# Kernel tuning notes

Hardware: AMD Instinct MI355X
Metric: run time of the kernel (lower is better)

The kernel has to match this reference:

```python
import jax, jax.numpy as jnp
import numpy as np

B = 8192
FL = 96      # feature_len
K = 3        # dynamic filter kernel size
NOUT = 2
EPS = 1e-5
P = (K - 1) // 2

def _lrelu(x):
    return jnp.where(x >= 0, x, 0.1 * x)

def _conv1d(x, w, b):
    # x: [b,1,L], w: [1,1,3], b: [1]; padding=1, stride=1
    y = jax.lax.conv_general_dilated(x, w, (1,), [(1, 1)], dimension_numbers=('NCH', 'OIH', 'NCH'))
    return y + b[None, :, None]

def _bn(y, g, be, m, v):
    # eval-mode BatchNorm1d with running stats
    return (y - m) / jnp.sqrt(v + EPS) * g + be


def setup_inputs() -> dict:
    key = jax.random.key(0)
    ks = jax.random.split(key, 40)
    d = {'x': jax.random.normal(ks[0], (B, 576), jnp.float32)}
    # trans_layer: 6 conv1d (1->1, k=3)
    for i in range(6):
        d[f'cw{i+1}'] = jax.random.normal(ks[1 + i], (1, 1, 3), jnp.float32) * 0.4
        d[f'cb{i+1}'] = jax.random.normal(ks[7 + i], (1,), jnp.float32) * 0.1
    # fusion_layer.de_dimen: Linear(FL -> K*K)
    d['de_W'] = jax.random.normal(ks[13], (K * K, FL), jnp.float32) * 0.1
    d['de_b'] = jnp.zeros((K * K,), jnp.float32)
    # reshape_layer: Linear(2*FL -> 3*FL) + BN
    d['rs_W'] = jax.random.normal(ks[14], (3 * FL, 2 * FL), jnp.float32) * 0.07
    d['rs_b'] = jnp.zeros((3 * FL,), jnp.float32)
    d['rs_g'] = 1.0 + 0.1 * jax.random.normal(ks[15], (3 * FL,), jnp.float32)
    d['rs_be'] = 0.1 * jax.random.normal(ks[16], (3 * FL,), jnp.float32)
    d['rs_m'] = 0.05 * jax.random.normal(ks[17], (3 * FL,), jnp.float32)
    d['rs_v'] = jax.random.uniform(ks[18], (3 * FL,), jnp.float32, 0.5, 1.5)
    # classifier_shallow: Linear(6*FL -> 3*FL) + BN + ReLU + Linear(3*FL -> NOUT)
    d['cl_W1'] = jax.random.normal(ks[19], (3 * FL, 6 * FL), jnp.float32) * 0.05
    d['cl_b1'] = jnp.zeros((3 * FL,), jnp.float32)
    d['cl_g'] = 1.0 + 0.1 * jax.random.normal(ks[20], (3 * FL,), jnp.float32)
    d['cl_be'] = 0.1 * jax.random.normal(ks[21], (3 * FL,), jnp.float32)
    d['cl_m'] = 0.05 * jax.random.normal(ks[22], (3 * FL,), jnp.float32)
    d['cl_v'] = jax.random.uniform(ks[23], (3 * FL,), jnp.float32, 0.5, 1.5)
    d['cl_W2'] = jax.random.normal(ks[24], (NOUT, 3 * FL), jnp.float32) * 0.05
    d['cl_b2'] = jnp.zeros((NOUT,), jnp.float32)
    return d


def reference(x, cw1, cb1, cw2, cb2, cw3, cb3, cw4, cb4, cw5, cb5, cw6, cb6,
              de_W, de_b, rs_W, rs_b, rs_g, rs_be, rs_m, rs_v,
              cl_W1, cl_b1, cl_g, cl_be, cl_m, cl_v, cl_W2, cl_b2):
    def trans(c):  # c: [b,1,3*FL] -> three [b,1,FL]
        s1, s2, s3 = c[..., :FL], c[..., FL:2 * FL], c[..., 2 * FL:]
        x1 = _lrelu(_conv1d(s1, cw1, cb1))
        x2 = _lrelu(_conv1d(s2, cw2, cb2))
        x3 = _lrelu(_conv1d(s3, cw3, cb3))
        return (_lrelu(_conv1d(x1, cw4, cb4)),
                _lrelu(_conv1d(x2, cw5, cb5)),
                _lrelu(_conv1d(x3, cw6, cb6)))

    def fusion(arm, x86, bert):  # each [b,1,FL]
        b = arm.shape[0]
        # c==1 so matmul(s_1^T, s_2) is a per-sample outer product: [b,FL,FL]
        m = _lrelu(jnp.einsum('bl,bm->blm', arm[:, 0], x86[:, 0]))
        # per-sample 3x3 dynamic filter from bert embedding
        s3 = _lrelu(bert[:, 0] @ de_W.T + de_b).reshape(b, 1, K, K)
        fe = jax.lax.conv_general_dilated(
            m.reshape(1, b, FL, FL), s3, (1, 1), [(P, P), (P, P)],
            feature_group_count=b, dimension_numbers=('NCHW', 'OIHW', 'NCHW'))
        fe = _lrelu(fe).reshape(b, FL, FL)
        # AvgPool1d(FL) == mean over last dim (and over rows for the permuted map)
        return jnp.concatenate([fe.mean(axis=2), fe.mean(axis=1)], axis=1)  # [b,2*FL]

    def resh(e):
        return _lrelu(_bn(e @ rs_W.T + rs_b, rs_g, rs_be, rs_m, rs_v))

    xu = x[:, None, :]  # unsqueeze(dim=1)
    c1, c2 = xu[..., :3 * FL], xu[..., 3 * FL:]
    e1 = resh(fusion(*trans(c1))) + c1[:, 0]
    e2 = resh(fusion(*trans(c2))) + c2[:, 0]
    ce = jnp.concatenate([e1, e2], axis=1)  # [b,6*FL]
    # Dropout is identity in eval mode
    h = jax.nn.relu(_bn(ce @ cl_W1.T + cl_b1, cl_g, cl_be, cl_m, cl_v))
    return h @ cl_W2.T + cl_b2  # [b,NOUT]
```

## Files before the change

kernel.cpp:

```cpp
#include <hip/hip_runtime.h>
#include <hip/hip_bf16.h>
#include <math.h>

#define FLn 96
#define SEG 288
#define EPRE_DIM 192
#define EPS_BN 1e-5f

typedef __attribute__((ext_vector_type(8))) short short8;
typedef __attribute__((ext_vector_type(4))) float floatx4;
typedef float v2f __attribute__((ext_vector_type(2)));

__device__ __forceinline__ float lrelu(float v) { return fmaxf(v, 0.1f * v); }
__device__ __forceinline__ short f2bf(float f) {
  __hip_bfloat16 h = __float2bfloat16(f);
  return *reinterpret_cast<short*>(&h);
}

#define O_CIN 0
#define O_ST1 288
#define O_APP 576
#define O_ANP 674
#define O_XPP 772
#define O_XNP 870
#define O_BERT 968
#define O_WKER 1064
#define O_ABF 0
#define O_BBF 384
#define O_RP 0
#define RPREG 1632
#define SLICE 3264

__global__ __launch_bounds__(128) void k1_persample(
    const float* __restrict__ x,
    const float* __restrict__ cw1, const float* __restrict__ cb1,
    const float* __restrict__ cw2, const float* __restrict__ cb2,
    const float* __restrict__ cw3, const float* __restrict__ cb3,
    const float* __restrict__ cw4, const float* __restrict__ cb4,
    const float* __restrict__ cw5, const float* __restrict__ cb5,
    const float* __restrict__ cw6, const float* __restrict__ cb6,
    const float* __restrict__ deW, const float* __restrict__ deb,
    const float* __restrict__ rsW, const float* __restrict__ clW1,
    short* __restrict__ wB2s, short* __restrict__ wB3s,
    short* __restrict__ epre_s) {
  __shared__ float S[SLICE];
  short* Ssh = (short*)S;
  const int tid = threadIdx.x;
  const int sw = tid >> 6;
  const int lane = tid & 63;
  const int quad = lane >> 4;
  const int l16 = lane & 15;
  const int unit = blockIdx.x;
  const float* xrow = x + (size_t)(unit >> 1) * 576 + (unit & 1) * 288;

  {
    int d = blockIdx.x * 128 + tid;
    if (d < 18 * 6 * 512) {
      int j = d & 7, ln = (d >> 3) & 63, t = d >> 9;
      int kf = t % 6, nf = t / 6;
      int n = nf * 16 + (ln & 15);
      int k = kf * 32 + (ln >> 4) * 8 + j;
      wB2s[d] = f2bf(rsW[n * 192 + k]);
    }
    if (d < 18 * 18 * 512) {
      int j = d & 7, ln = (d >> 3) & 63, t = d >> 9;
      int kf = t % 18, nt = t / 18;
      int n = nt * 16 + (ln & 15);
      int k = kf * 32 + (ln >> 4) * 8 + j;
      wB3s[d] = f2bf(clW1[n * 576 + k]);
    }
  }

  const float a0w0 = cw1[0], a0w1 = cw1[1], a0w2 = cw1[2], a0b = cb1[0];
  const float a1w0 = cw2[0], a1w1 = cw2[1], a1w2 = cw2[2], a1b = cb2[0];
  const float a2w0 = cw3[0], a2w1 = cw3[1], a2w2 = cw3[2], a2b = cb3[0];
  const float b0w0 = cw4[0], b0w1 = cw4[1], b0w2 = cw4[2], b0b = cb4[0];
  const float b1w0 = cw5[0], b1w1 = cw5[1], b1w2 = cw5[2], b1b = cb5[0];
  const float b2w0 = cw6[0], b2w1 = cw6[1], b2w2 = cw6[2], b2b = cb6[0];

  for (int t4 = tid; t4 < 72; t4 += 128)
    *(float4*)&S[O_CIN + 4 * t4] = ((const float4*)xrow)[t4];
  if (tid < 8) S[576 + 98 * (tid >> 1) + (tid & 1) * 97] = 0.f;
  __syncthreads();

  for (int t = tid; t < SEG; t += 128) {
    bool g1 = t >= 96, g2 = t >= 192;
    float wa = g2 ? a2w0 : (g1 ? a1w0 : a0w0);
    float wb = g2 ? a2w1 : (g1 ? a1w1 : a0w1);
    float wc = g2 ? a2w2 : (g1 ? a1w2 : a0w2);
    float bb = g2 ? a2b  : (g1 ? a1b  : a0b);
    int p = t - (g2 ? 192 : (g1 ? 96 : 0));
    float l = p > 0 ? S[O_CIN + t - 1] : 0.f;
    float m = S[O_CIN + t];
    float r = p < FLn - 1 ? S[O_CIN + t + 1] : 0.f;
    S[O_ST1 + t] = lrelu(fmaf(wa, l, fmaf(wb, m, fmaf(wc, r, bb))));
  }
  __syncthreads();
  for (int t = tid; t < SEG; t += 128) {
    bool g1 = t >= 96, g2 = t >= 192;
    float wa = g2 ? b2w0 : (g1 ? b1w0 : b0w0);
    float wb = g2 ? b2w1 : (g1 ? b1w1 : b0w1);
    float wc = g2 ? b2w2 : (g1 ? b1w2 : b0w2);
    float bb = g2 ? b2b  : (g1 ? b1b  : b0b);
    int p = t - (g2 ? 192 : (g1 ? 96 : 0));
    float l = p > 0 ? S[O_ST1 + t - 1] : 0.f;
    float m = S[O_ST1 + t];
    float r = p < FLn - 1 ? S[O_ST1 + t + 1] : 0.f;
    float v = lrelu(fmaf(wa, l, fmaf(wb, m, fmaf(wc, r, bb))));
    if (!g1) {
      S[O_APP + 1 + p] = fmaxf(v, 0.1f * v);
      S[O_ANP + 1 + p] = fminf(v, 0.1f * v);
    } else if (!g2) {
      S[O_XPP + 1 + p] = fmaxf(v, 0.f);
      S[O_XNP + 1 + p] = fminf(v, 0.f);
    } else {
      S[O_BERT + p] = v;
    }
  }
  __syncthreads();

  if (sw == 0) {
    if (quad < 3) {
      float bv[6];
#pragma unroll
      for (int k = 0; k < 6; ++k) bv[k] = S[O_BERT + l16 + 16 * k];
#pragma unroll
      for (int oi = 0; oi < 3; ++oi) {
        int o = quad * 3 + oi;
        float p = 0.f;
#pragma unroll
        for (int k = 0; k < 6; ++k) p = fmaf(bv[k], deW[o * 96 + l16 + 16 * k], p);
        p += __shfl_xor(p, 1, 16);
        p += __shfl_xor(p, 2, 16);
        p += __shfl_xor(p, 4, 16);
        p += __shfl_xor(p, 8, 16);
        if (l16 == 0) S[O_WKER + o] = lrelu(p + deb[o]);
      }
    }
  } else {
    for (int m = lane; m < 96; m += 64) {
      short8 a;
      a[0] = f2bf(S[O_APP + m]);
      a[1] = f2bf(S[O_APP + m + 1]);
      a[2] = f2bf(S[O_APP + m + 2]);
      a[3] = f2bf(S[O_ANP + m]);
      a[4] = f2bf(S[O_ANP + m + 1]);
      a[5] = f2bf(S[O_ANP + m + 2]);
      a[6] = 0; a[7] = 0;
      *(short8*)&Ssh[2 * O_ABF + m * 8] = a;
    }
  }
  __syncthreads();

  {
    float w9[9];
#pragma unroll
    for (int q = 0; q < 9; ++q) w9[q] = 0.25f * S[O_WKER + q];
    for (int t = tid; t < 96; t += 128) {
      float xp0 = S[O_XPP + t], xp1 = S[O_XPP + t + 1], xp2 = S[O_XPP + t + 2];
      float xn0 = S[O_XNP + t], xn1 = S[O_XNP + t + 1], xn2 = S[O_XNP + t + 2];
      short8 b;
#pragma unroll
      for (int d = 0; d < 3; ++d) {
        float cp = fmaf(w9[3 * d], xp0, fmaf(w9[3 * d + 1], xp1, w9[3 * d + 2] * xp2));
        float cn = fmaf(w9[3 * d], xn0, fmaf(w9[3 * d + 1], xn1, w9[3 * d + 2] * xn2));
        b[d] = f2bf(cp);
        b[3 + d] = f2bf(cn);
      }
      b[6] = 0; b[7] = 0;
      *(short8*)&Ssh[2 * O_BBF + t * 8] = b;
    }
  }
  __syncthreads();

  short8 aF[6];
#pragma unroll
  for (int mt = 0; mt < 6; ++mt)
    aF[mt] = *(const short8*)&Ssh[2 * O_ABF + (mt * 16 + l16) * 8];

  v2f rp2[6][2];
#pragma unroll
  for (int mt = 0; mt < 6; ++mt) {
    rp2[mt][0] = (v2f){0.f, 0.f};
    rp2[mt][1] = (v2f){0.f, 0.f};
  }
  float cs[3];

#pragma unroll
  for (int si = 0; si < 3; ++si) {
    const int s = 3 * sw + si;
    short8 bF = *(const short8*)&Ssh[2 * O_BBF + (s * 16 + l16) * 8];
    floatx4 accv[6];
#pragma unroll
    for (int mt = 0; mt < 6; ++mt)
      accv[mt] = __builtin_amdgcn_mfma_f32_16x16x32_bf16(
          aF[mt], bF, (floatx4){0.f, 0.f, 0.f, 0.f}, 0, 0, 0);
    v2f csl = (v2f){0.f, 0.f};
#pragma unroll
    for (int mt = 0; mt < 6; ++mt) {
      v2f lo = (v2f){accv[mt][0], accv[mt][1]};
      v2f hi = (v2f){accv[mt][2], accv[mt][3]};
      v2f tl = 0.1f * lo;
      v2f th = 0.1f * hi;
      v2f fl, fh;
      fl.x = fmaxf(lo.x, tl.x); fl.y = fmaxf(lo.y, tl.y);
      fh.x = fmaxf(hi.x, th.x); fh.y = fmaxf(hi.y, th.y);
      rp2[mt][0] += fl;
      rp2[mt][1] += fh;
      csl += fl + fh;
    }
    cs[si] = csl.x + csl.y;
  }
  __syncthreads();

#pragma unroll
  for (int mt = 0; mt < 6; ++mt)
    *(float4*)&S[O_RP + sw * RPREG + (quad * 6 + mt) * 68 + l16 * 4] =
        make_float4(rp2[mt][0].x, rp2[mt][0].y, rp2[mt][1].x, rp2[mt][1].y);
  __syncthreads();

  const int g = unit >> 4;
  const int u15 = unit & 15;
  short* eb = epre_s + (size_t)g * 6 * 512;
  for (int i = tid; i < 96; i += 128) {
    int gg = ((i >> 2) & 3) * 6 + (i >> 4);
    int r = i & 3;
    float s = 0.f;
#pragma unroll
    for (int l = 0; l < 16; ++l)
      s += S[O_RP + gg * 68 + l * 4 + r] + S[O_RP + RPREG + gg * 68 + l * 4 + r];
    int kf = i >> 5, rem = i & 31, q = rem >> 3, j = rem & 7;
    eb[kf * 512 + (q * 16 + u15) * 8 + j] = f2bf(s * (1.f / FLn));
  }
#pragma unroll
  for (int si = 0; si < 3; ++si) {
    float v = cs[si];
    v += __shfl_xor(v, 16, 64);
    v += __shfl_xor(v, 32, 64);
    if (quad == 0) {
      int kidx = 96 + (3 * sw + si) * 16 + l16;
      int kf = kidx >> 5, rem = kidx & 31, q = rem >> 3, j = rem & 7;
      eb[kf * 512 + (q * 16 + u15) * 8 + j] = f2bf(v * (1.f / FLn));
    }
  }
}

__global__ __launch_bounds__(512) void k6_fused_tail(
    const short* __restrict__ epre_s, const short* __restrict__ wB2s,
    const short* __restrict__ wB3s, const float* __restrict__ x,
    const float* __restrict__ rsb, const float* __restrict__ rsg,
    const float* __restrict__ rsbe, const float* __restrict__ rsm,
    const float* __restrict__ rsv,
    const float* __restrict__ clb1, const float* __restrict__ clg,
    const float* __restrict__ clbe, const float* __restrict__ clm,
    const float* __restrict__ clv,
    const float* __restrict__ clW2, const float* __restrict__ clb2,
    float* __restrict__ out) {
  __shared__ short ceT[16 * 584];
  __shared__ float scr[8 * 32];
  const int tid = threadIdx.x;
  const int w = tid >> 6;
  const int lane = tid & 63;
  const int quad = lane >> 4;
  const int l16 = lane & 15;
  const int s0 = blockIdx.x * 16;

  const int mt = w & 1;
  const int ng = w >> 1;
  short8 aF[6];
  {
    const short* arow = epre_s + (size_t)(blockIdx.x * 2 + mt) * 6 * 512 + lane * 8;
#pragma unroll
    for (int kf = 0; kf < 6; ++kf) aF[kf] = *(const short8*)(arow + kf * 512);
  }

  for (int nf = ng; nf < 18; nf += 4) {
    const short* brow = wB2s + (size_t)nf * 6 * 512 + lane * 8;
    floatx4 acc = (floatx4){0.f, 0.f, 0.f, 0.f};
#pragma unroll
    for (int kf = 0; kf < 6; ++kf) {
      short8 bF = *(const short8*)(brow + kf * 512);
      acc = __builtin_amdgcn_mfma_f32_16x16x32_bf16(aF[kf], bF, acc, 0, 0, 0);
    }
    const int n = nf * 16 + l16;
    const float sc = rsg[n] * rsqrtf(rsv[n] + EPS_BN);
    const float vb = rsb[n], mu = rsm[n], vbe = rsbe[n];
#pragma unroll
    for (int r = 0; r < 4; ++r) {
      int um = mt * 16 + quad * 4 + r;
      int trow = um >> 1;
      int cc = (um & 1) * 288 + n;
      float y = acc[r] + vb;
      float o = (y - mu) * sc + vbe;
      float e = lrelu(o) + x[(size_t)(s0 + trow) * 576 + cc];
      ceT[trow * 584 + cc] = f2bf(e);
    }
  }
  __syncthreads();

  float p0[4], p1[4];
#pragma unroll
  for (int r = 0; r < 4; ++r) { p0[r] = 0.f; p1[r] = 0.f; }

  for (int nt = w; nt < 18; nt += 8) {
    const short* brow = wB3s + (size_t)nt * 18 * 512 + lane * 8;
    floatx4 acc = (floatx4){0.f, 0.f, 0.f, 0.f};
#pragma unroll
    for (int kf = 0; kf < 18; ++kf) {
      short8 cF = *(const short8*)&ceT[l16 * 584 + kf * 32 + quad * 8];
      short8 bF = *(const short8*)(brow + kf * 512);
      acc = __builtin_amdgcn_mfma_f32_16x16x32_bf16(cF, bF, acc, 0, 0, 0);
    }
    const int n = nt * 16 + l16;
    const float sc = clg[n] * rsqrtf(clv[n] + EPS_BN);
    const float vb = clb1[n], mu = clm[n], vbe = clbe[n];
    const float w2a = clW2[n], w2b = clW2[288 + n];
#pragma unroll
    for (int r = 0; r < 4; ++r) {
      float y = acc[r] + vb;
      float hh = fmaxf((y - mu) * sc + vbe, 0.f);
      p0[r] = fmaf(hh, w2a, p0[r]);
      p1[r] = fmaf(hh, w2b, p1[r]);
    }
  }
#pragma unroll
  for (int r = 0; r < 4; ++r) {
#pragma unroll
    for (int off = 1; off < 16; off <<= 1) {
      p0[r] += __shfl_xor(p0[r], off, 64);
      p1[r] += __shfl_xor(p1[r], off, 64);
    }
  }
  if (l16 == 0) {
#pragma unroll
    for (int r = 0; r < 4; ++r) {
      scr[w * 32 + (quad * 4 + r) * 2 + 0] = p0[r];
      scr[w * 32 + (quad * 4 + r) * 2 + 1] = p1[r];
    }
  }
  __syncthreads();
  if (tid < 32) {
    int row = tid >> 1, o = tid & 1;
    float s = 0.f;
#pragma unroll
    for (int g = 0; g < 8; ++g) s += scr[g * 32 + row * 2 + o];
    out[(size_t)(s0 + row) * 2 + o] = s + clb2[o];
  }
}

extern "C" void kernel_launch(void* const* d_in, const int* in_sizes, int n_in,
                              void* d_out, int out_size, void* d_ws, size_t ws_size,
                              hipStream_t stream) {
  const float* x   = (const float*)d_in[0];
  const float* cw1 = (const float*)d_in[1];  const float* cb1 = (const float*)d_in[2];
  const float* cw2 = (const float*)d_in[3];  const float* cb2 = (const float*)d_in[4];
  const float* cw3 = (const float*)d_in[5];  const float* cb3 = (const float*)d_in[6];
  const float* cw4 = (const float*)d_in[7];  const float* cb4 = (const float*)d_in[8];
  const float* cw5 = (const float*)d_in[9];  const float* cb5 = (const float*)d_in[10];
  const float* cw6 = (const float*)d_in[11]; const float* cb6 = (const float*)d_in[12];
  const float* deW = (const float*)d_in[13]; const float* deb = (const float*)d_in[14];
  const float* rsW = (const float*)d_in[15]; const float* rsb = (const float*)d_in[16];
  const float* rsg = (const float*)d_in[17]; const float* rsbe = (const float*)d_in[18];
  const float* rsm = (const float*)d_in[19]; const float* rsv = (const float*)d_in[20];
  const float* clW1 = (const float*)d_in[21]; const float* clb1 = (const float*)d_in[22];
  const float* clg = (const float*)d_in[23]; const float* clbe = (const float*)d_in[24];
  const float* clm = (const float*)d_in[25]; const float* clv = (const float*)d_in[26];
  const float* clW2 = (const float*)d_in[27]; const float* clb2 = (const float*)d_in[28];

  short* ws     = (short*)d_ws;
  short* epre_s = ws;
  short* wB2s   = ws + 16384 * 192;
  short* wB3s   = wB2s + 18 * 6 * 512;

  hipLaunchKernelGGL(k1_persample, dim3(16384), dim3(128), 0, stream, x,
                     cw1, cb1, cw2, cb2, cw3, cb3, cw4, cb4, cw5, cb5, cw6, cb6,
                     deW, deb, rsW, clW1, wB2s, wB3s, epre_s);
  hipLaunchKernelGGL(k6_fused_tail, dim3(512), dim3(512), 0, stream,
                     epre_s, wB2s, wB3s, x,
                     rsb, rsg, rsbe, rsm, rsv,
                     clb1, clg, clbe, clm, clv,
                     clW2, clb2, (float*)d_out);
}
```

Baseline: 191.3 us.

## Rebalance per-sample kernel to three waves and halve tail block size

```diff
diff --git a/kernel.cpp b/kernel.cpp
--- a/kernel.cpp
+++ b/kernel.cpp
@@ -29,9 +29,9 @@
 #define O_BBF 384
 #define O_RP 0
 #define RPREG 1632
-#define SLICE 3264
-
-__global__ __launch_bounds__(128) void k1_persample(
+#define SLICE 4896
+
+__global__ __launch_bounds__(192) void k1_persample(
     const float* __restrict__ x,
     const float* __restrict__ cw1, const float* __restrict__ cb1,
     const float* __restrict__ cw2, const float* __restrict__ cb2,
@@ -54,7 +54,7 @@
   const float* xrow = x + (size_t)(unit >> 1) * 576 + (unit & 1) * 288;
 
   {
-    int d = blockIdx.x * 128 + tid;
+    int d = blockIdx.x * 192 + tid;
     if (d < 18 * 6 * 512) {
       int j = d & 7, ln = (d >> 3) & 63, t = d >> 9;
       int kf = t % 6, nf = t / 6;
@@ -78,12 +78,14 @@
   const float b1w0 = cw5[0], b1w1 = cw5[1], b1w2 = cw5[2], b1b = cb5[0];
   const float b2w0 = cw6[0], b2w1 = cw6[1], b2w2 = cw6[2], b2b = cb6[0];
 
-  for (int t4 = tid; t4 < 72; t4 += 128)
-    *(float4*)&S[O_CIN + 4 * t4] = ((const float4*)xrow)[t4];
-  if (tid < 8) S[576 + 98 * (tid >> 1) + (tid & 1) * 97] = 0.f;
-  __syncthreads();
-
-  for (int t = tid; t < SEG; t += 128) {
+  if (tid < 72) *(float4*)&S[O_CIN + 4 * tid] = ((const float4*)xrow)[tid];
+  if (tid >= 72 && tid < 80) {
+    int z = tid - 72;
+    S[576 + 98 * (z >> 1) + (z & 1) * 97] = 0.f;
+  }
+  __syncthreads();
+
+  for (int t = tid; t < SEG; t += 192) {
     bool g1 = t >= 96, g2 = t >= 192;
     float wa = g2 ? a2w0 : (g1 ? a1w0 : a0w0);
     float wb = g2 ? a2w1 : (g1 ? a1w1 : a0w1);
@@ -96,7 +98,7 @@
     S[O_ST1 + t] = lrelu(fmaf(wa, l, fmaf(wb, m, fmaf(wc, r, bb))));
   }
   __syncthreads();
-  for (int t = tid; t < SEG; t += 128) {
+  for (int t = tid; t < SEG; t += 192) {
     bool g1 = t >= 96, g2 = t >= 192;
     float wa = g2 ? b2w0 : (g1 ? b1w0 : b0w0);
     float wb = g2 ? b2w1 : (g1 ? b1w1 : b0w1);
@@ -138,7 +140,8 @@
       }
     }
   } else {
-    for (int m = lane; m < 96; m += 64) {
+    int m = lane + 64 * (sw - 1);
+    if (m < 96) {
       short8 a;
       a[0] = f2bf(S[O_APP + m]);
       a[1] = f2bf(S[O_APP + m + 1]);
@@ -152,24 +155,23 @@
   }
   __syncthreads();
 
-  {
+  if (tid < 96) {
     float w9[9];
 #pragma unroll
     for (int q = 0; q < 9; ++q) w9[q] = 0.25f * S[O_WKER + q];
-    for (int t = tid; t < 96; t += 128) {
-      float xp0 = S[O_XPP + t], xp1 = S[O_XPP + t + 1], xp2 = S[O_XPP + t + 2];
-      float xn0 = S[O_XNP + t], xn1 = S[O_XNP + t + 1], xn2 = S[O_XNP + t + 2];
-      short8 b;
-#pragma unroll
-      for (int d = 0; d < 3; ++d) {
-        float cp = fmaf(w9[3 * d], xp0, fmaf(w9[3 * d + 1], xp1, w9[3 * d + 2] * xp2));
-        float cn = fmaf(w9[3 * d], xn0, fmaf(w9[3 * d + 1], xn1, w9[3 * d + 2] * xn2));
-        b[d] = f2bf(cp);
-        b[3 + d] = f2bf(cn);
-      }
-      b[6] = 0; b[7] = 0;
-      *(short8*)&Ssh[2 * O_BBF + t * 8] = b;
-    }
+    int t = tid;
+    float xp0 = S[O_XPP + t], xp1 = S[O_XPP + t + 1], xp2 = S[O_XPP + t + 2];
+    float xn0 = S[O_XNP + t], xn1 = S[O_XNP + t + 1], xn2 = S[O_XNP + t + 2];
+    short8 b;
+#pragma unroll
+    for (int d = 0; d < 3; ++d) {
+      float cp = fmaf(w9[3 * d], xp0, fmaf(w9[3 * d + 1], xp1, w9[3 * d + 2] * xp2));
+      float cn = fmaf(w9[3 * d], xn0, fmaf(w9[3 * d + 1], xn1, w9[3 * d + 2] * xn2));
+      b[d] = f2bf(cp);
+      b[3 + d] = f2bf(cn);
+    }
+    b[6] = 0; b[7] = 0;
+    *(short8*)&Ssh[2 * O_BBF + t * 8] = b;
   }
   __syncthreads();
 
@@ -184,11 +186,11 @@
     rp2[mt][0] = (v2f){0.f, 0.f};
     rp2[mt][1] = (v2f){0.f, 0.f};
   }
-  float cs[3];
-
-#pragma unroll
-  for (int si = 0; si < 3; ++si) {
-    const int s = 3 * sw + si;
+  float cs[2];
+
+#pragma unroll
+  for (int si = 0; si < 2; ++si) {
+    const int s = 2 * sw + si;
     short8 bF = *(const short8*)&Ssh[2 * O_BBF + (s * 16 + l16) * 8];
     floatx4 accv[6];
 #pragma unroll
@@ -222,30 +224,33 @@
   const int g = unit >> 4;
   const int u15 = unit & 15;
   short* eb = epre_s + (size_t)g * 6 * 512;
-  for (int i = tid; i < 96; i += 128) {
+  if (tid < 96) {
+    int i = tid;
     int gg = ((i >> 2) & 3) * 6 + (i >> 4);
     int r = i & 3;
     float s = 0.f;
 #pragma unroll
     for (int l = 0; l < 16; ++l)
-      s += S[O_RP + gg * 68 + l * 4 + r] + S[O_RP + RPREG + gg * 68 + l * 4 + r];
+      s += S[O_RP + gg * 68 + l * 4 + r] +
+           S[O_RP + RPREG + gg * 68 + l * 4 + r] +
+           S[O_RP + 2 * RPREG + gg * 68 + l * 4 + r];
     int kf = i >> 5, rem = i & 31, q = rem >> 3, j = rem & 7;
     eb[kf * 512 + (q * 16 + u15) * 8 + j] = f2bf(s * (1.f / FLn));
   }
 #pragma unroll
-  for (int si = 0; si < 3; ++si) {
+  for (int si = 0; si < 2; ++si) {
     float v = cs[si];
     v += __shfl_xor(v, 16, 64);
     v += __shfl_xor(v, 32, 64);
     if (quad == 0) {
-      int kidx = 96 + (3 * sw + si) * 16 + l16;
+      int kidx = 96 + (2 * sw + si) * 16 + l16;
       int kf = kidx >> 5, rem = kidx & 31, q = rem >> 3, j = rem & 7;
       eb[kf * 512 + (q * 16 + u15) * 8 + j] = f2bf(v * (1.f / FLn));
     }
   }
 }
 
-__global__ __launch_bounds__(512) void k6_fused_tail(
+__global__ __launch_bounds__(256) void k6_fused_tail(
     const short* __restrict__ epre_s, const short* __restrict__ wB2s,
     const short* __restrict__ wB3s, const float* __restrict__ x,
     const float* __restrict__ rsb, const float* __restrict__ rsg,
@@ -257,24 +262,22 @@
     const float* __restrict__ clW2, const float* __restrict__ clb2,
     float* __restrict__ out) {
   __shared__ short ceT[16 * 584];
-  __shared__ float scr[8 * 32];
+  __shared__ float scr[4 * 16];
   const int tid = threadIdx.x;
   const int w = tid >> 6;
   const int lane = tid & 63;
   const int quad = lane >> 4;
   const int l16 = lane & 15;
-  const int s0 = blockIdx.x * 16;
-
-  const int mt = w & 1;
-  const int ng = w >> 1;
+  const int s0 = blockIdx.x * 8;
+
   short8 aF[6];
   {
-    const short* arow = epre_s + (size_t)(blockIdx.x * 2 + mt) * 6 * 512 + lane * 8;
+    const short* arow = epre_s + (size_t)blockIdx.x * 6 * 512 + lane * 8;
 #pragma unroll
     for (int kf = 0; kf < 6; ++kf) aF[kf] = *(const short8*)(arow + kf * 512);
   }
 
-  for (int nf = ng; nf < 18; nf += 4) {
+  for (int nf = w; nf < 18; nf += 4) {
     const short* brow = wB2s + (size_t)nf * 6 * 512 + lane * 8;
     floatx4 acc = (floatx4){0.f, 0.f, 0.f, 0.f};
 #pragma unroll
@@ -287,7 +290,7 @@
     const float vb = rsb[n], mu = rsm[n], vbe = rsbe[n];
 #pragma unroll
     for (int r = 0; r < 4; ++r) {
-      int um = mt * 16 + quad * 4 + r;
+      int um = quad * 4 + r;
       int trow = um >> 1;
       int cc = (um & 1) * 288 + n;
       float y = acc[r] + vb;
@@ -302,14 +305,21 @@
 #pragma unroll
   for (int r = 0; r < 4; ++r) { p0[r] = 0.f; p1[r] = 0.f; }
 
-  for (int nt = w; nt < 18; nt += 8) {
+  for (int nt = w; nt < 18; nt += 4) {
     const short* brow = wB3s + (size_t)nt * 18 * 512 + lane * 8;
-    floatx4 acc = (floatx4){0.f, 0.f, 0.f, 0.f};
-#pragma unroll
-    for (int kf = 0; kf < 18; ++kf) {
+    floatx4 accA = (floatx4){0.f, 0.f, 0.f, 0.f};
+    floatx4 accB = (floatx4){0.f, 0.f, 0.f, 0.f};
+#pragma unroll
+    for (int kf = 0; kf < 9; ++kf) {
       short8 cF = *(const short8*)&ceT[l16 * 584 + kf * 32 + quad * 8];
       short8 bF = *(const short8*)(brow + kf * 512);
-      acc = __builtin_amdgcn_mfma_f32_16x16x32_bf16(cF, bF, acc, 0, 0, 0);
+      accA = __builtin_amdgcn_mfma_f32_16x16x32_bf16(cF, bF, accA, 0, 0, 0);
+    }
+#pragma unroll
+    for (int kf = 9; kf < 18; ++kf) {
+      short8 cF = *(const short8*)&ceT[l16 * 584 + kf * 32 + quad * 8];
+      short8 bF = *(const short8*)(brow + kf * 512);
+      accB = __builtin_amdgcn_mfma_f32_16x16x32_bf16(cF, bF, accB, 0, 0, 0);
     }
     const int n = nt * 16 + l16;
     const float sc = clg[n] * rsqrtf(clv[n] + EPS_BN);
@@ -317,7 +327,7 @@
     const float w2a = clW2[n], w2b = clW2[288 + n];
 #pragma unroll
     for (int r = 0; r < 4; ++r) {
-      float y = acc[r] + vb;
+      float y = accA[r] + accB[r] + vb;
       float hh = fmaxf((y - mu) * sc + vbe, 0.f);
       p0[r] = fmaf(hh, w2a, p0[r]);
       p1[r] = fmaf(hh, w2b, p1[r]);
@@ -331,19 +341,18 @@
       p1[r] += __shfl_xor(p1[r], off, 64);
     }
   }
-  if (l16 == 0) {
+  if (l16 == 0 && quad < 2) {
 #pragma unroll
     for (int r = 0; r < 4; ++r) {
-      scr[w * 32 + (quad * 4 + r) * 2 + 0] = p0[r];
-      scr[w * 32 + (quad * 4 + r) * 2 + 1] = p1[r];
-    }
-  }
-  __syncthreads();
-  if (tid < 32) {
+      scr[w * 16 + (quad * 4 + r) * 2 + 0] = p0[r];
+      scr[w * 16 + (quad * 4 + r) * 2 + 1] = p1[r];
+    }
+  }
+  __syncthreads();
+  if (tid < 16) {
     int row = tid >> 1, o = tid & 1;
-    float s = 0.f;
-#pragma unroll
-    for (int g = 0; g < 8; ++g) s += scr[g * 32 + row * 2 + o];
+    float s = scr[row * 2 + o] + scr[16 + row * 2 + o] +
+              scr[32 + row * 2 + o] + scr[48 + row * 2 + o];
     out[(size_t)(s0 + row) * 2 + o] = s + clb2[o];
   }
 }
@@ -372,10 +381,10 @@
   short* wB2s   = ws + 16384 * 192;
   short* wB3s   = wB2s + 18 * 6 * 512;
 
-  hipLaunchKernelGGL(k1_persample, dim3(16384), dim3(128), 0, stream, x,
+  hipLaunchKernelGGL(k1_persample, dim3(16384), dim3(192), 0, stream, x,
                      cw1, cb1, cw2, cb2, cw3, cb3, cw4, cb4, cw5, cb5, cw6, cb6,
                      deW, deb, rsW, clW1, wB2s, wB3s, epre_s);
-  hipLaunchKernelGGL(k6_fused_tail, dim3(512), dim3(512), 0, stream,
+  hipLaunchKernelGGL(k6_fused_tail, dim3(1024), dim3(256), 0, stream,
                      epre_s, wB2s, wB3s, x,
                      rsb, rsg, rsbe, rsm, rsv,
                      clb1, clg, clbe, clm, clv,
```

After: 205.5 us. +7.4%, slower.
